# Performance work log

Hardware: AMD Instinct MI355X
Metric: run time of the kernel (lower is better)

## Reference

```python
import jax, jax.numpy as jnp
import numpy as np

B, S, D, HD, H = 4, 4096, 1024, 120, 1  # batch, seq, d_model, h_dim, heads (code only runs for h=1)
EPS = 1e-12  # F.normalize eps


def setup_inputs() -> dict:
    key = jax.random.key(0)
    k0, k1, k2, k3 = jax.random.split(key, 4)
    query = jax.random.normal(k0, (B, S, D), dtype=jnp.float32)
    key_t = jax.random.normal(k1, (B, S, D), dtype=jnp.float32)  # unused by forward, but a required arg
    # q_linear: Linear(d_model, h_dim*h) -> weight [HD, D], bias [HD]
    Wq = jax.random.normal(k2, (HD * H, D), dtype=jnp.float32) * np.float32(1.0 / np.sqrt(D))
    bq = jnp.zeros((HD * H,), dtype=jnp.float32)
    # weight_tensor: xavier_uniform on shape (h, d_k) = (1, 120)
    bound = np.float32(np.sqrt(6.0 / (H + HD * H)))
    weight_tensor = jax.random.uniform(k3, (H, HD * H), dtype=jnp.float32, minval=-bound, maxval=bound)
    return {"query": query, "key": key_t, "Wq": Wq, "bq": bq, "weight_tensor": weight_tensor}


def reference(query, key, Wq, bq, weight_tensor):
    # context = q_linear(query).view(B, -1, h_dim); with h=1 this is [B, S, HD]
    context = jnp.einsum('bsd,hd->bsh', query, Wq) + bq  # [B,S,HD]
    # context_fc = context.unsqueeze(0) * weight_tensor[h,1,1,d_k] -> [h,B,S,HD]
    ctx = context[None, :, :, :] * weight_tensor[:, None, None, :]  # [h,B,S,HD]
    # F.normalize(p=2, dim=-1): x / max(||x||, eps)
    nrm = jnp.sqrt(jnp.sum(ctx * ctx, axis=-1, keepdims=True))
    ctx_n = ctx / jnp.maximum(nrm, EPS)
    # per-head gram matrix then mean over heads -> [B,S,S]
    scores = jnp.einsum('hbsd,hbtd->hbst', ctx_n, ctx_n).mean(axis=0)
    # mask=None path; dropout is identity in eval mode
    return jax.nn.softmax(scores, axis=-1)
```

## Files before the change

kernel.cpp:

```cpp
#include <hip/hip_runtime.h>
#include <hip/hip_fp16.h>

#define BATCH   4
#define SEQ     4096
#define DMODEL  1024
#define HDIM    120
#define NPAD    128
#define ROWS_TOTAL (BATCH * SEQ)
#define TPB     256

typedef float f32x4 __attribute__((ext_vector_type(4)));
typedef short s16x8 __attribute__((ext_vector_type(8)));

#define FRAG_PER_B ((size_t)TPB * 4 * 64)

static __device__ __forceinline__ unsigned short f2bf(float f) {
    unsigned u = __float_as_uint(f);
    u += 0x7FFFu + ((u >> 16) & 1u);
    return (unsigned short)(u >> 16);
}
static __device__ __forceinline__ s16x8 pack2x4(f32x4 lo, f32x4 hi) {
    s16x8 r;
#pragma unroll
    for (int i = 0; i < 4; ++i) r[i] = (short)f2bf(lo[i]);
#pragma unroll
    for (int i = 0; i < 4; ++i) r[4 + i] = (short)f2bf(hi[i]);
    return r;
}

__global__ __launch_bounds__(64)
void wq_frag_kernel(const float* __restrict__ Wq, const float* __restrict__ wt,
                    s16x8* __restrict__ WF)
{
    const int lane = threadIdx.x;
    const int l15  = lane & 15;
    const int l4   = lane >> 4;
    const int ct   = blockIdx.x >> 5;
    const int ks   = blockIdx.x & 31;
    const int col  = ct * 16 + l15;

    f32x4 lo = (f32x4){0.f,0.f,0.f,0.f}, hi = lo;
    if (col < HDIM) {
        const float w = wt[col];
        const float* src = Wq + (size_t)col * DMODEL + ks * 32 + l4 * 8;
        lo = *(const f32x4*)(src);
        hi = *(const f32x4*)(src + 4);
#pragma unroll
        for (int i = 0; i < 4; ++i) { lo[i] *= w; hi[i] *= w; }
    }
    WF[((size_t)(ct * 32 + ks)) * 64 + lane] = pack2x4(lo, hi);
}

__global__ __launch_bounds__(512)
void ctx_norm_kernel(const float* __restrict__ query,
                     const s16x8* __restrict__ WF,
                     const float* __restrict__ bq,
                     const float* __restrict__ wt,
                     s16x8* __restrict__ F)
{
    __shared__ unsigned short lA[2][64 * 40];
    __shared__ float lsq[64][2];
    __shared__ unsigned short lt[64][136];

    const int tid  = threadIdx.x;
    const int lane = tid & 63;
    const int wv   = tid >> 6;
    const int wr   = wv & 3;
    const int wc   = wv >> 2;
    const int l15  = lane & 15;
    const int l4   = lane >> 4;
    const int row0 = blockIdx.x * 64;

    const int arow = tid >> 3, achk = tid & 7;
    const float* aload = query + (size_t)(row0 + arow) * DMODEL + achk * 4;

    f32x4 acc[4];
#pragma unroll
    for (int n = 0; n < 4; ++n) acc[n] = (f32x4){0.f,0.f,0.f,0.f};

    f32x4 pr = *(const f32x4*)(aload);
    {
        const unsigned u0 = (unsigned)f2bf(pr[0]) | ((unsigned)f2bf(pr[1]) << 16);
        const unsigned u1 = (unsigned)f2bf(pr[2]) | ((unsigned)f2bf(pr[3]) << 16);
        *(uint2*)&lA[0][arow * 40 + achk * 4] = make_uint2(u0, u1);
    }

    for (int ks = 0; ks < 32; ++ks) {
        __syncthreads();
        if (ks + 1 < 32) pr = *(const f32x4*)(aload + (ks + 1) * 32);
        const int buf = ks & 1;
        const s16x8 a = *(const s16x8*)&lA[buf][(wr * 16 + l15) * 40 + l4 * 8];
#pragma unroll
        for (int n = 0; n < 4; ++n) {
            const s16x8 bfr = WF[((size_t)((wc * 4 + n) * 32 + ks)) * 64 + lane];
            acc[n] = __builtin_amdgcn_mfma_f32_16x16x32_bf16(a, bfr, acc[n], 0, 0, 0);
        }
        if (ks + 1 < 32) {
            const unsigned u0 = (unsigned)f2bf(pr[0]) | ((unsigned)f2bf(pr[1]) << 16);
            const unsigned u1 = (unsigned)f2bf(pr[2]) | ((unsigned)f2bf(pr[3]) << 16);
            *(uint2*)&lA[buf ^ 1][arow * 40 + achk * 4] = make_uint2(u0, u1);
        }
    }

    float sumsq[4] = {0.f,0.f,0.f,0.f};
#pragma unroll
    for (int n = 0; n < 4; ++n) {
        const int col = wc * 64 + n * 16 + l15;
        const float bqv = (col < HDIM) ? bq[col] * wt[col] : 0.f;
#pragma unroll
        for (int r = 0; r < 4; ++r) {
            const float v = acc[n][r] + bqv;
            acc[n][r] = v;
            sumsq[r] += v * v;
        }
    }
#pragma unroll
    for (int r = 0; r < 4; ++r) {
        float s = sumsq[r];
        s += __shfl_xor(s, 1);
        s += __shfl_xor(s, 2);
        s += __shfl_xor(s, 4);
        s += __shfl_xor(s, 8);
        sumsq[r] = s;
    }
    if (l15 == 0) {
#pragma unroll
        for (int r = 0; r < 4; ++r)
            lsq[wr * 16 + l4 * 4 + r][wc] = sumsq[r];
    }
    __syncthreads();
#pragma unroll
    for (int r = 0; r < 4; ++r) {
        const int lr = wr * 16 + l4 * 4 + r;
        const float s = lsq[lr][0] + lsq[lr][1];
        const float rinv = 1.f / fmaxf(sqrtf(s), 1e-12f);
#pragma unroll
        for (int n = 0; n < 4; ++n)
            lt[lr][wc * 64 + n * 16 + l15] = f2bf(acc[n][r] * rinv);
    }
    __syncthreads();
#pragma unroll
    for (int q = 0; q < 2; ++q) {
        const int idx = wv * 2 + q;
        const int tl  = idx >> 2;
        const int k4  = idx & 3;
        const s16x8 fr = *(const s16x8*)&lt[tl * 16 + l15][k4 * 32 + l4 * 8];
        F[((size_t)(blockIdx.x * 4 + tl) * 4 + k4) * 64 + lane] = fr;
    }
}

#define LOADT(dst, t) { const s16x8* _p = base + (size_t)(t) * 256;            \
    dst[0] = _p[0]; dst[1] = _p[64]; dst[2] = _p[128]; dst[3] = _p[192]; }

#define COMPT(src, t) { f32x4 _a = (f32x4){0.f, 0.f, 0.f, 0.f};                \
    _a = __builtin_amdgcn_mfma_f32_16x16x32_bf16(src[0], rfrag[0], _a, 0,0,0); \
    _a = __builtin_amdgcn_mfma_f32_16x16x32_bf16(src[1], rfrag[1], _a, 0,0,0); \
    _a = __builtin_amdgcn_mfma_f32_16x16x32_bf16(src[2], rfrag[2], _a, 0,0,0); \
    _a = __builtin_amdgcn_mfma_f32_16x16x32_bf16(src[3], rfrag[3], _a, 0,0,0); \
    const float _e0 = __expf(_a[0]), _e1 = __expf(_a[1]);                      \
    const float _e2 = __expf(_a[2]), _e3 = __expf(_a[3]);                      \
    rs += (_e0 + _e1) + (_e2 + _e3);                                           \
    const __half2 _h01 = __floats2half2_rn(_e0, _e1);                          \
    const __half2 _h23 = __floats2half2_rn(_e2, _e3);                          \
    unsigned _byte = (unsigned)(l15 * 8192 + cg * 512 + (t) * 32 + l4 * 8);    \
    _byte ^= (unsigned)(l15 << 4);                                             \
    *(uint2*)(lsbase + _byte) =                                                \
        make_uint2(*(const unsigned*)&_h01, *(const unsigned*)&_h23); }

__global__ __launch_bounds__(1024)
void gram_fused_kernel(const s16x8* __restrict__ F, float* __restrict__ out)
{
    __shared__ unsigned short lsE[16][4096];
    __shared__ float lsum[16][16];

    const int tid  = threadIdx.x;
    const int lane = tid & 63;
    const int cg   = tid >> 6;
    const int l15  = lane & 15;
    const int l4   = lane >> 4;
    char* lsbase = (char*)&lsE[0][0];

    const int u    = ((blockIdx.x & 7) << 7) | (blockIdx.x >> 3);
    const int b    = u >> 8;
    const int tr   = u & 255;
    const s16x8* Fb = F + (size_t)b * FRAG_PER_B;

    s16x8 rfrag[4];
#pragma unroll
    for (int ks = 0; ks < 4; ++ks) rfrag[ks] = Fb[((size_t)tr * 4 + ks) * 64 + lane];

    const s16x8* base = Fb + (size_t)(cg * 16) * 256 + lane;

    float rs = 0.f;
    s16x8 cA[4], cB[4], cC[4];
    LOADT(cA, 0)
    LOADT(cB, 1)
    LOADT(cC, 2)
#pragma unroll
    for (int i = 0; i < 6; ++i) {
        const int t = i * 3;
        { COMPT(cA, t)           if (t + 3 < 16) LOADT(cA, t + 3) }
        if (t + 1 < 16) { COMPT(cB, t + 1) if (t + 4 < 16) LOADT(cB, t + 4) }
        if (t + 2 < 16) { COMPT(cC, t + 2) if (t + 5 < 16) LOADT(cC, t + 5) }
    }

    rs += __shfl_xor(rs, 16);
    rs += __shfl_xor(rs, 32);
    if (lane < 16) lsum[lane][cg] = rs;
    __syncthreads();

    float s = 0.f;
#pragma unroll
    for (int w = 0; w < 16; ++w) s += lsum[cg][w];
    const float rv = 1.f / s;

    float* ob = out + ((size_t)b * SEQ + tr * 16 + cg) * SEQ;
    const unsigned swz = (unsigned)(cg << 4);
#pragma unroll
    for (int it = 0; it < 16; ++it) {
        const unsigned sbyte = (unsigned)(cg * 8192 + it * 512 + lane * 8) ^ swz;
        const uint2 d = *(const uint2*)(lsbase + sbyte);
        const float2 f01 = __half22float2(*(const __half2*)&d.x);
        const float2 f23 = __half22float2(*(const __half2*)&d.y);
        f32x4 pv;
        pv[0] = f01.x * rv;
        pv[1] = f01.y * rv;
        pv[2] = f23.x * rv;
        pv[3] = f23.y * rv;
        __builtin_nontemporal_store(pv, (f32x4*)(ob + it * 256 + lane * 4));
    }
}

extern "C" void kernel_launch(void* const* d_in, const int* in_sizes, int n_in,
                              void* d_out, int out_size, void* d_ws, size_t ws_size,
                              hipStream_t stream)
{
    const float* query = (const float*)d_in[0];
    const float* Wq    = (const float*)d_in[2];
    const float* bq    = (const float*)d_in[3];
    const float* wt    = (const float*)d_in[4];
    float* out = (float*)d_out;
    s16x8* F  = (s16x8*)d_ws;
    s16x8* WF = (s16x8*)((char*)d_ws + (size_t)4 * 1024 * 1024);

    wq_frag_kernel<<<dim3(256), dim3(64), 0, stream>>>(Wq, wt, WF);
    ctx_norm_kernel<<<dim3(ROWS_TOTAL / 64), dim3(512), 0, stream>>>(query, WF, bq, wt, F);
    gram_fused_kernel<<<dim3(BATCH * TPB), dim3(1024), 0, stream>>>(F, out);
}
```

Baseline: 109.7 us.

## Hold exp tiles in registers and stage output through a small LDS buffer

```diff
diff --git a/kernel.cpp b/kernel.cpp
--- a/kernel.cpp
+++ b/kernel.cpp
@@ -5,7 +5,6 @@
 #define SEQ     4096
 #define DMODEL  1024
 #define HDIM    120
-#define NPAD    128
 #define ROWS_TOTAL (BATCH * SEQ)
 #define TPB     256
 
@@ -149,10 +148,10 @@
     }
 }
 
-#define LOADT(dst, t) { const s16x8* _p = base + (size_t)(t) * 256;            \
+#define LOADT5(dst, t) { const s16x8* _p = base + (size_t)(t) * 2048;          \
     dst[0] = _p[0]; dst[1] = _p[64]; dst[2] = _p[128]; dst[3] = _p[192]; }
 
-#define COMPT(src, t) { f32x4 _a = (f32x4){0.f, 0.f, 0.f, 0.f};                \
+#define COMPT5(src, t) { f32x4 _a = (f32x4){0.f, 0.f, 0.f, 0.f};               \
     _a = __builtin_amdgcn_mfma_f32_16x16x32_bf16(src[0], rfrag[0], _a, 0,0,0); \
     _a = __builtin_amdgcn_mfma_f32_16x16x32_bf16(src[1], rfrag[1], _a, 0,0,0); \
     _a = __builtin_amdgcn_mfma_f32_16x16x32_bf16(src[2], rfrag[2], _a, 0,0,0); \
@@ -162,23 +161,21 @@
     rs += (_e0 + _e1) + (_e2 + _e3);                                           \
     const __half2 _h01 = __floats2half2_rn(_e0, _e1);                          \
     const __half2 _h23 = __floats2half2_rn(_e2, _e3);                          \
-    unsigned _byte = (unsigned)(l15 * 8192 + cg * 512 + (t) * 32 + l4 * 8);    \
-    _byte ^= (unsigned)(l15 << 4);                                             \
-    *(uint2*)(lsbase + _byte) =                                                \
-        make_uint2(*(const unsigned*)&_h01, *(const unsigned*)&_h23); }
-
-__global__ __launch_bounds__(1024)
+    ex0[t] = *(const unsigned*)&_h01;                                          \
+    ex1[t] = *(const unsigned*)&_h23; }
+
+__global__ __launch_bounds__(512, 4)
 void gram_fused_kernel(const s16x8* __restrict__ F, float* __restrict__ out)
 {
-    __shared__ unsigned short lsE[16][4096];
-    __shared__ float lsum[16][16];
+    __shared__ unsigned short lsB[16 * 1024];
+    __shared__ float lsum[16][8];
 
     const int tid  = threadIdx.x;
     const int lane = tid & 63;
     const int cg   = tid >> 6;
     const int l15  = lane & 15;
     const int l4   = lane >> 4;
-    char* lsbase = (char*)&lsE[0][0];
+    char* lsb = (char*)&lsB[0];
 
     const int u    = ((blockIdx.x & 7) << 7) | (blockIdx.x >> 3);
     const int b    = u >> 8;
@@ -189,19 +186,18 @@
 #pragma unroll
     for (int ks = 0; ks < 4; ++ks) rfrag[ks] = Fb[((size_t)tr * 4 + ks) * 64 + lane];
 
-    const s16x8* base = Fb + (size_t)(cg * 16) * 256 + lane;
-
+    const s16x8* base = Fb + (size_t)cg * 256 + lane;
+
+    unsigned ex0[32], ex1[32];
     float rs = 0.f;
-    s16x8 cA[4], cB[4], cC[4];
-    LOADT(cA, 0)
-    LOADT(cB, 1)
-    LOADT(cC, 2)
-#pragma unroll
-    for (int i = 0; i < 6; ++i) {
-        const int t = i * 3;
-        { COMPT(cA, t)           if (t + 3 < 16) LOADT(cA, t + 3) }
-        if (t + 1 < 16) { COMPT(cB, t + 1) if (t + 4 < 16) LOADT(cB, t + 4) }
-        if (t + 2 < 16) { COMPT(cC, t + 2) if (t + 5 < 16) LOADT(cC, t + 5) }
+    s16x8 cf0[4], cf1[4];
+
+    LOADT5(cf0, 0)
+    LOADT5(cf1, 1)
+#pragma unroll
+    for (int i = 0; i < 16; ++i) {
+        { COMPT5(cf0, 2 * i)     if (2 * i + 2 < 32) LOADT5(cf0, 2 * i + 2) }
+        { COMPT5(cf1, 2 * i + 1) if (2 * i + 3 < 32) LOADT5(cf1, 2 * i + 3) }
     }
 
     rs += __shfl_xor(rs, 16);
@@ -209,25 +205,49 @@
     if (lane < 16) lsum[lane][cg] = rs;
     __syncthreads();
 
-    float s = 0.f;
-#pragma unroll
-    for (int w = 0; w < 16; ++w) s += lsum[cg][w];
-    const float rv = 1.f / s;
-
-    float* ob = out + ((size_t)b * SEQ + tr * 16 + cg) * SEQ;
-    const unsigned swz = (unsigned)(cg << 4);
-#pragma unroll
-    for (int it = 0; it < 16; ++it) {
-        const unsigned sbyte = (unsigned)(cg * 8192 + it * 512 + lane * 8) ^ swz;
-        const uint2 d = *(const uint2*)(lsbase + sbyte);
-        const float2 f01 = __half22float2(*(const __half2*)&d.x);
-        const float2 f23 = __half22float2(*(const __half2*)&d.y);
-        f32x4 pv;
-        pv[0] = f01.x * rv;
-        pv[1] = f01.y * rv;
-        pv[2] = f23.x * rv;
-        pv[3] = f23.y * rv;
-        __builtin_nontemporal_store(pv, (f32x4*)(ob + it * 256 + lane * 4));
+    const int r0 = cg * 2, r1 = cg * 2 + 1;
+    float s0 = 0.f, s1 = 0.f;
+#pragma unroll
+    for (int w = 0; w < 8; ++w) { s0 += lsum[r0][w]; s1 += lsum[r1][w]; }
+    const float rv0 = 1.f / s0;
+    const float rv1 = 1.f / s1;
+
+    float* ob0 = out + ((size_t)b * SEQ + tr * 16 + r0) * SEQ;
+    float* ob1 = out + ((size_t)b * SEQ + tr * 16 + r1) * SEQ;
+    const unsigned wswz = (unsigned)((l15 & 7) << 4);
+    const unsigned rswz0 = (unsigned)((r0 & 7) << 4);
+    const unsigned rswz1 = (unsigned)((r1 & 7) << 4);
+
+#pragma unroll
+    for (int c = 0; c < 4; ++c) {
+        if (c > 0) __syncthreads();
+#pragma unroll
+        for (int i = 0; i < 8; ++i) {
+            const int t = c * 8 + i;
+            const unsigned byte = ((unsigned)(l15 * 2048 + (i * 8 + cg) * 32 + l4 * 8)) ^ wswz;
+            *(uint2*)(lsb + byte) = make_uint2(ex0[t], ex1[t]);
+        }
+        __syncthreads();
+#pragma unroll
+        for (int it = 0; it < 4; ++it) {
+            const unsigned byA = ((unsigned)(r0 * 2048 + it * 512 + lane * 8)) ^ rswz0;
+            const uint2 dA = *(const uint2*)(lsb + byA);
+            const float2 a01 = __half22float2(*(const __half2*)&dA.x);
+            const float2 a23 = __half22float2(*(const __half2*)&dA.y);
+            f32x4 pA;
+            pA[0] = a01.x * rv0; pA[1] = a01.y * rv0;
+            pA[2] = a23.x * rv0; pA[3] = a23.y * rv0;
+            __builtin_nontemporal_store(pA, (f32x4*)(ob0 + c * 1024 + it * 256 + lane * 4));
+
+            const unsigned byB = ((unsigned)(r1 * 2048 + it * 512 + lane * 8)) ^ rswz1;
+            const uint2 dB = *(const uint2*)(lsb + byB);
+            const float2 b01 = __half22float2(*(const __half2*)&dB.x);
+            const float2 b23 = __half22float2(*(const __half2*)&dB.y);
+            f32x4 pB;
+            pB[0] = b01.x * rv1; pB[1] = b01.y * rv1;
+            pB[2] = b23.x * rv1; pB[3] = b23.y * rv1;
+            __builtin_nontemporal_store(pB, (f32x4*)(ob1 + c * 1024 + it * 256 + lane * 4));
+        }
     }
 }
 
@@ -245,5 +265,5 @@
 
     wq_frag_kernel<<<dim3(256), dim3(64), 0, stream>>>(Wq, wt, WF);
     ctx_norm_kernel<<<dim3(ROWS_TOTAL / 64), dim3(512), 0, stream>>>(query, WF, bq, wt, F);
-    gram_fused_kernel<<<dim3(BATCH * TPB), dim3(1024), 0, stream>>>(F, out);
-}
+    gram_fused_kernel<<<dim3(BATCH * TPB), dim3(512), 0, stream>>>(F, out);
+}
```

Result: slower. 123.4 us (+12.5%).

## Halve row tile in ctx_norm to 32 rows, double blocks and K-slab depth

Applied to the files above, without the earlier changes.

```diff
diff --git a/kernel.cpp b/kernel.cpp
--- a/kernel.cpp
+++ b/kernel.cpp
@@ -5,7 +5,6 @@
 #define SEQ     4096
 #define DMODEL  1024
 #define HDIM    120
-#define NPAD    128
 #define ROWS_TOTAL (BATCH * SEQ)
 #define TPB     256
 
@@ -58,54 +57,57 @@
                      const float* __restrict__ wt,
                      s16x8* __restrict__ F)
 {
-    __shared__ unsigned short lA[2][64 * 40];
-    __shared__ float lsq[64][2];
-    __shared__ unsigned short lt[64][136];
+    __shared__ unsigned short lA[2][32 * 72];
+    __shared__ float lsq[32][4];
+    __shared__ unsigned short lt[32][136];
 
     const int tid  = threadIdx.x;
     const int lane = tid & 63;
     const int wv   = tid >> 6;
-    const int wr   = wv & 3;
-    const int wc   = wv >> 2;
+    const int wr   = wv & 1;
+    const int wc   = wv >> 1;
     const int l15  = lane & 15;
     const int l4   = lane >> 4;
-    const int row0 = blockIdx.x * 64;
-
-    const int arow = tid >> 3, achk = tid & 7;
+    const int row0 = blockIdx.x * 32;
+
+    const int arow = tid >> 4;
+    const int achk = tid & 15;
     const float* aload = query + (size_t)(row0 + arow) * DMODEL + achk * 4;
 
-    f32x4 acc[4];
-#pragma unroll
-    for (int n = 0; n < 4; ++n) acc[n] = (f32x4){0.f,0.f,0.f,0.f};
+    f32x4 acc[2];
+#pragma unroll
+    for (int n = 0; n < 2; ++n) acc[n] = (f32x4){0.f,0.f,0.f,0.f};
+
+    auto stage = [&](int buf, const f32x4& v) {
+        const unsigned u0 = (unsigned)f2bf(v[0]) | ((unsigned)f2bf(v[1]) << 16);
+        const unsigned u1 = (unsigned)f2bf(v[2]) | ((unsigned)f2bf(v[3]) << 16);
+        *(uint2*)&lA[buf][arow * 72 + achk * 4] = make_uint2(u0, u1);
+    };
 
     f32x4 pr = *(const f32x4*)(aload);
-    {
-        const unsigned u0 = (unsigned)f2bf(pr[0]) | ((unsigned)f2bf(pr[1]) << 16);
-        const unsigned u1 = (unsigned)f2bf(pr[2]) | ((unsigned)f2bf(pr[3]) << 16);
-        *(uint2*)&lA[0][arow * 40 + achk * 4] = make_uint2(u0, u1);
-    }
-
-    for (int ks = 0; ks < 32; ++ks) {
+    stage(0, pr);
+
+    for (int slab = 0; slab < 16; ++slab) {
         __syncthreads();
-        if (ks + 1 < 32) pr = *(const f32x4*)(aload + (ks + 1) * 32);
-        const int buf = ks & 1;
-        const s16x8 a = *(const s16x8*)&lA[buf][(wr * 16 + l15) * 40 + l4 * 8];
-#pragma unroll
-        for (int n = 0; n < 4; ++n) {
-            const s16x8 bfr = WF[((size_t)((wc * 4 + n) * 32 + ks)) * 64 + lane];
-            acc[n] = __builtin_amdgcn_mfma_f32_16x16x32_bf16(a, bfr, acc[n], 0, 0, 0);
+        if (slab + 1 < 16) pr = *(const f32x4*)(aload + (slab + 1) * 64);
+        const int buf = slab & 1;
+#pragma unroll
+        for (int ks2 = 0; ks2 < 2; ++ks2) {
+            const int ks = slab * 2 + ks2;
+            const s16x8 a = *(const s16x8*)&lA[buf][(wr * 16 + l15) * 72 + ks2 * 32 + l4 * 8];
+#pragma unroll
+            for (int n = 0; n < 2; ++n) {
+                const s16x8 bfr = WF[((size_t)((wc * 2 + n) * 32 + ks)) * 64 + lane];
+                acc[n] = __builtin_amdgcn_mfma_f32_16x16x32_bf16(a, bfr, acc[n], 0, 0, 0);
+            }
         }
-        if (ks + 1 < 32) {
-            const unsigned u0 = (unsigned)f2bf(pr[0]) | ((unsigned)f2bf(pr[1]) << 16);
-            const unsigned u1 = (unsigned)f2bf(pr[2]) | ((unsigned)f2bf(pr[3]) << 16);
-            *(uint2*)&lA[buf ^ 1][arow * 40 + achk * 4] = make_uint2(u0, u1);
-        }
+        if (slab + 1 < 16) stage(buf ^ 1, pr);
     }
 
     float sumsq[4] = {0.f,0.f,0.f,0.f};
 #pragma unroll
-    for (int n = 0; n < 4; ++n) {
-        const int col = wc * 64 + n * 16 + l15;
+    for (int n = 0; n < 2; ++n) {
+        const int col = wc * 32 + n * 16 + l15;
         const float bqv = (col < HDIM) ? bq[col] * wt[col] : 0.f;
 #pragma unroll
         for (int r = 0; r < 4; ++r) {
@@ -132,20 +134,18 @@
 #pragma unroll
     for (int r = 0; r < 4; ++r) {
         const int lr = wr * 16 + l4 * 4 + r;
-        const float s = lsq[lr][0] + lsq[lr][1];
+        const float s = lsq[lr][0] + lsq[lr][1] + lsq[lr][2] + lsq[lr][3];
         const float rinv = 1.f / fmaxf(sqrtf(s), 1e-12f);
 #pragma unroll
-        for (int n = 0; n < 4; ++n)
-            lt[lr][wc * 64 + n * 16 + l15] = f2bf(acc[n][r] * rinv);
+        for (int n = 0; n < 2; ++n)
+            lt[lr][wc * 32 + n * 16 + l15] = f2bf(acc[n][r] * rinv);
     }
     __syncthreads();
-#pragma unroll
-    for (int q = 0; q < 2; ++q) {
-        const int idx = wv * 2 + q;
-        const int tl  = idx >> 2;
-        const int k4  = idx & 3;
+    {
+        const int tl = wv >> 2;
+        const int k4 = wv & 3;
         const s16x8 fr = *(const s16x8*)&lt[tl * 16 + l15][k4 * 32 + l4 * 8];
-        F[((size_t)(blockIdx.x * 4 + tl) * 4 + k4) * 64 + lane] = fr;
+        F[((size_t)(blockIdx.x * 2 + tl) * 4 + k4) * 64 + lane] = fr;
     }
 }
 
@@ -244,6 +244,6 @@
     s16x8* WF = (s16x8*)((char*)d_ws + (size_t)4 * 1024 * 1024);
 
     wq_frag_kernel<<<dim3(256), dim3(64), 0, stream>>>(Wq, wt, WF);
-    ctx_norm_kernel<<<dim3(ROWS_TOTAL / 64), dim3(512), 0, stream>>>(query, WF, bq, wt, F);
+    ctx_norm_kernel<<<dim3(ROWS_TOTAL / 32), dim3(512), 0, stream>>>(query, WF, bq, wt, F);
     gram_fused_kernel<<<dim3(BATCH * TPB), dim3(1024), 0, stream>>>(F, out);
 }
```

Result: faster. 101.0 us, median of 2 (-7.9%).
